# Kernel optimization log

Measured on AMD Instinct MI355X. Metric: run time of the kernel, lower is better.

The kernel has to match this reference:

```python
import jax, jax.numpy as jnp
import numpy as np

D = 1024       # d_model
H = 16         # total heads
HD = 64        # k_dim per head
HL = 8         # local heads (block-local attention)
STRIDE = 128   # block size
C = 32         # summary columns per block for global heads
DFF = 4096
EPS = 1e-6
NEG = -1e9


def layernorm(x, g, b):
    mu = jnp.mean(x, axis=-1, keepdims=True)
    var = jnp.mean(jnp.square(x - mu), axis=-1, keepdims=True)
    return g * (x - mu) / jnp.sqrt(var + EPS) + b


def setup_inputs() -> dict:
    key = jax.random.key(0)
    ks = jax.random.split(key, 16)
    B, S = 4, 4096
    s = 0.02
    inp = {
        "src": jax.random.normal(ks[0], (B, S, D), jnp.float32),
        "input_mask": jnp.ones((B, S), dtype=bool),
        "Wq": jax.random.normal(ks[1], (D, H * HD), jnp.float32) * s,
        "bq": jnp.zeros((H * HD,), jnp.float32),
        "Wk": jax.random.normal(ks[2], (D, H * HD), jnp.float32) * s,
        "bk": jnp.zeros((H * HD,), jnp.float32),
        "Wv": jax.random.normal(ks[3], (D, H * HD), jnp.float32) * s,
        "bv": jnp.zeros((H * HD,), jnp.float32),
        "Wo": jax.random.normal(ks[4], (H * HD, D), jnp.float32) * s,
        "bo": jnp.zeros((D,), jnp.float32),
        "ln1_g": jnp.ones((D,), jnp.float32),
        "ln1_b": jnp.zeros((D,), jnp.float32),
        "W1": jax.random.normal(ks[5], (D, DFF), jnp.float32) * s,
        "b1": jnp.zeros((DFF,), jnp.float32),
        "W2": jax.random.normal(ks[6], (DFF, D), jnp.float32) * s,
        "b2": jnp.zeros((D,), jnp.float32),
        "ln2_g": jnp.ones((D,), jnp.float32),
        "ln2_b": jnp.zeros((D,), jnp.float32),
    }
    return inp


def sparse_attention(src, input_mask, Wq, bq, Wk, bk, Wv, bv, Wo, bo):
    B, S, _ = src.shape
    nb = S // STRIDE
    scale = HD ** -0.5
    q = (src @ Wq + bq).reshape(B, S, H, HD)
    k = (src @ Wk + bk).reshape(B, S, H, HD)
    v = (src @ Wv + bv).reshape(B, S, H, HD)

    # ---- local heads: attend within their own block of length STRIDE ----
    ql = q[:, :, :HL].reshape(B, nb, STRIDE, HL, HD)
    kl = k[:, :, :HL].reshape(B, nb, STRIDE, HL, HD)
    vl = v[:, :, :HL].reshape(B, nb, STRIDE, HL, HD)
    sl = jnp.einsum('bnqhd,bnkhd->bnhqk', ql, kl) * scale
    mloc = input_mask.reshape(B, nb, 1, 1, STRIDE)
    sl = jnp.where(mloc, sl, NEG)
    al = jax.nn.softmax(sl, axis=-1)
    ol = jnp.einsum('bnhqk,bnkhd->bnqhd', al, vl).reshape(B, S, HL, HD)

    # ---- global heads: attend to last C positions of every block (fixed pattern) ----
    idx = np.nonzero(np.arange(S) % STRIDE >= STRIDE - C)[0]  # static, nb*C keys
    kg = k[:, idx, HL:]                        # [B, nb*C, HG, HD]
    vg = v[:, idx, HL:]
    sg = jnp.einsum('bqhd,bkhd->bhqk', q[:, :, HL:], kg) * scale
    mg = input_mask[:, idx][:, None, None, :]
    sg = jnp.where(mg, sg, NEG)
    ag = jax.nn.softmax(sg, axis=-1)
    og = jnp.einsum('bhqk,bkhd->bqhd', ag, vg)  # [B, S, HG, HD]

    out = jnp.concatenate([ol, og], axis=2).reshape(B, S, H * HD)
    return out @ Wo + bo


def reference(src, input_mask, Wq, bq, Wk, bk, Wv, bv, Wo, bo,
              ln1_g, ln1_b, W1, b1, W2, b2, ln2_g, ln2_b):
    temp = sparse_attention(src, input_mask, Wq, bq, Wk, bk, Wv, bv, Wo, bo)
    attn = layernorm(src + temp, ln1_g, ln1_b)
    ffn = jax.nn.relu(attn @ W1 + b1) @ W2 + b2
    state = layernorm(attn + ffn, ln2_g, ln2_b)
    return state
```

## Files before the change

### kernel.cpp

```cpp
#include <hip/hip_runtime.h>
#include <hip/hip_bf16.h>
#include <stdint.h>


typedef unsigned short bf16_t;
typedef __attribute__((ext_vector_type(8))) short short8;
typedef __attribute__((ext_vector_type(4))) float v4f;

static __device__ __forceinline__ unsigned short f2b(float f) {
    unsigned int x = __float_as_uint(f);
    x += 0x7fffu + ((x >> 16) & 1u);
    return (unsigned short)(x >> 16);
}
static __device__ __forceinline__ float b2f(unsigned short u) {
    return __uint_as_float(((unsigned int)u) << 16);
}

static __device__ __forceinline__ void gload16(const void* g, void* l) {
    __builtin_amdgcn_global_load_lds(
        (const __attribute__((address_space(1))) uint32_t*)g,
        (__attribute__((address_space(3))) uint32_t*)l, 16, 0, 0);
}

template<int N>
static __device__ __forceinline__ void vmwait() {
    asm volatile("s_waitcnt vmcnt(%0)" :: "n"(N) : "memory");
}
static __device__ __forceinline__ void lgkmwait0() {
    asm volatile("s_waitcnt lgkmcnt(0)" ::: "memory");
}


__global__ __launch_bounds__(256) void transpose_convert(
    const float* __restrict__ W, bf16_t* __restrict__ Wt, int K, int N) {
    __shared__ float tile[32][33];
    int n0 = blockIdx.x * 32, k0 = blockIdx.y * 32;
    int tx = threadIdx.x, ty = threadIdx.y;
    for (int i = ty; i < 32; i += 8)
        tile[i][tx] = W[(size_t)(k0 + i) * N + n0 + tx];
    __syncthreads();
    for (int i = ty; i < 32; i += 8)
        Wt[(size_t)(n0 + i) * K + k0 + tx] = f2b(tile[tx][i]);
}

__global__ __launch_bounds__(256) void f32_to_bf16_vec(
    const float* __restrict__ in, bf16_t* __restrict__ out, int n4) {
    int i = blockIdx.x * blockDim.x + threadIdx.x;
    if (i >= n4) return;
    float4 v = ((const float4*)in)[i];
    uint2 p;
    p.x = (unsigned)f2b(v.x) | ((unsigned)f2b(v.y) << 16);
    p.y = (unsigned)f2b(v.z) | ((unsigned)f2b(v.w) << 16);
    ((uint2*)out)[i] = p;
}

template<bool GLOBAL>
__global__ __launch_bounds__(256) void v_transpose(
    const bf16_t* __restrict__ qkv, bf16_t* __restrict__ vt, int ntok) {
    __shared__ bf16_t tile[4096];
    int tb = blockIdx.x, h = blockIdx.y, b = blockIdx.z;
    int t = threadIdx.x;
    size_t src = (size_t)b * 4096 * 3072 + (size_t)(GLOBAL ? h + 8 : h) * 64 + 2048;
    for (int u = t; u < 512; u += 256) {
        int row = u >> 3, g = u & 7;
        int lt = tb * 64 + row;
        int tok = GLOBAL ? ((lt >> 5) * 128 + 96 + (lt & 31)) : lt;
        short8 vrow = *(const short8*)(qkv + src + (size_t)tok * 3072 + g * 8);
        *(short8*)&tile[(row * 8 + (g ^ (row >> 3))) * 8] = vrow;
    }
    __syncthreads();
    for (int u = t; u < 512; u += 256) {
        int d = u >> 3, t8g = u & 7;
        short8 vcol;
#pragma unroll
        for (int j = 0; j < 8; ++j) {
            int row = t8g * 8 + j;
            vcol[j] = tile[(row * 8 + ((d >> 3) ^ (row >> 3))) * 8 + (d & 7)];
        }
        *(short8*)(vt + ((size_t)(b * 8 + h) * 64 + d) * ntok + (size_t)tb * 64 + t8g * 8) = vcol;
    }
}

template<int BN>
__global__ __launch_bounds__(512, 2) void gemm_bt(
    const bf16_t* __restrict__ A, const bf16_t* __restrict__ Bt,
    const float* __restrict__ bias, const float* __restrict__ bias2,
    const float* __restrict__ bias3, const float* __restrict__ resf,
    const bf16_t* __restrict__ resb, float* __restrict__ Cf,
    bf16_t* __restrict__ Cb, int N, int K, int relu) {
    constexpr int N_REP = BN / 64;
    constexpr int BLD = BN / 128;
    constexpr int LPT = 2 + BLD;
    constexpr int ASH = 8192;
    constexpr int TSH = ASH + BN * 32;
    __shared__ bf16_t lds[4][TSH];

    int t = threadIdx.x;
    int lane = t & 63;
    int wave = t >> 6;
    int wm = (wave >> 2) * 128;
    int wn = (wave & 3) * (BN / 4);
    int m0 = blockIdx.x * 256, n0 = blockIdx.y * BN;

    size_t aoff[2]; int adst[2];
#pragma unroll
    for (int p = 0; p < 2; ++p) {
        int u = p * 512 + t;
        int row = ((u >> 6) << 4) + (lane & 15);
        int kk = ((u >> 4) & 3) * 8;
        aoff[p] = (size_t)(m0 + row) * K + kk;
        adst[p] = (u & ~63) * 8;
    }
    size_t boff[BLD]; int bdst[BLD];
#pragma unroll
    for (int p = 0; p < BLD; ++p) {
        int u = p * 512 + t;
        int row = ((u >> 6) << 4) + (lane & 15);
        int kk = ((u >> 4) & 3) * 8;
        boff[p] = (size_t)(n0 + row) * K + kk;
        bdst[p] = (u & ~63) * 8;
    }

    auto stage = [&](int buf, int kt) {
        int k0 = kt * 32;
#pragma unroll
        for (int p = 0; p < 2; ++p)
            gload16(A + aoff[p] + k0, &lds[buf][adst[p]]);
#pragma unroll
        for (int p = 0; p < BLD; ++p)
            gload16(Bt + boff[p] + k0, &lds[buf][ASH + bdst[p]]);
    };

    v4f acc[8][N_REP];
#pragma unroll
    for (int i = 0; i < 8; ++i)
#pragma unroll
        for (int j = 0; j < N_REP; ++j) acc[i][j] = {0.f, 0.f, 0.f, 0.f};

    int NT = K >> 5;
    stage(0, 0); stage(1, 1); stage(2, 2);

    int aro = (wm >> 4) * 512 + lane * 8;
    int bro = ASH + (wn >> 4) * 512 + lane * 8;

    short8 fA0[8], fB0[N_REP], fA1[8], fB1[N_REP];

    auto prep = [&](int it, short8 (&gA)[8], short8 (&gB)[N_REP]) {
        if (it + 1 < NT) {
            if (it + 2 < NT) vmwait<LPT>();
            else vmwait<0>();
            __builtin_amdgcn_s_barrier();
            __builtin_amdgcn_sched_barrier(0);
            int nb = (it + 1) & 3;
#pragma unroll
            for (int i = 0; i < 8; ++i)
                gA[i] = *(const short8*)&lds[nb][aro + i * 512];
#pragma unroll
            for (int j = 0; j < N_REP; ++j)
                gB[j] = *(const short8*)&lds[nb][bro + j * 512];
            if (it + 3 < NT) stage((it + 3) & 3, it + 3);
            __builtin_amdgcn_sched_barrier(0);
        }
    };
    auto mstep = [&](short8 (&gA)[8], short8 (&gB)[N_REP]) {
        __builtin_amdgcn_s_setprio(1);
#pragma unroll
        for (int i = 0; i < 8; ++i)
#pragma unroll
            for (int j = 0; j < N_REP; ++j)
                acc[i][j] = __builtin_amdgcn_mfma_f32_16x16x32_bf16(gA[i], gB[j], acc[i][j], 0, 0, 0);
        __builtin_amdgcn_s_setprio(0);
    };

    vmwait<2 * LPT>();
    __builtin_amdgcn_s_barrier();
    __builtin_amdgcn_sched_barrier(0);
#pragma unroll
    for (int i = 0; i < 8; ++i) fA0[i] = *(const short8*)&lds[0][aro + i * 512];
#pragma unroll
    for (int j = 0; j < N_REP; ++j) fB0[j] = *(const short8*)&lds[0][bro + j * 512];

    for (int it = 0; it < NT; it += 2) {
        prep(it, fA1, fB1);
        mstep(fA0, fB0);
        prep(it + 1, fA0, fB0);
        mstep(fA1, fB1);
    }

    int qrow = (lane >> 4) * 4;
    int c15 = lane & 15;
#pragma unroll
    for (int i = 0; i < 8; ++i) {
#pragma unroll
        for (int j = 0; j < N_REP; ++j) {
            int col = n0 + wn + j * 16 + c15;
            float bval;
            if (bias2) {
                int seg = col >> 10;
                const float* bp = seg == 0 ? bias : (seg == 1 ? bias2 : bias3);
                bval = bp[col & 1023];
            } else {
                bval = bias[col];
            }
#pragma unroll
            for (int r = 0; r < 4; ++r) {
                int row = m0 + wm + i * 16 + qrow + r;
                size_t idx = (size_t)row * N + col;
                float val = acc[i][j][r] + bval;
                if (resf) val += resf[idx];
                if (resb) val += b2f(resb[idx]);
                if (relu) val = fmaxf(val, 0.f);
                if (Cf) Cf[idx] = val;
                if (Cb) Cb[idx] = f2b(val);
            }
        }
    }
}

template<int NCHUNK, bool GLOBAL>
__global__ __launch_bounds__(256) void mfma_attn(
    const bf16_t* __restrict__ qkv, const bf16_t* __restrict__ vt,
    bf16_t* __restrict__ o, int head_base) {
    __shared__ bf16_t buf[32768];
    bf16_t* ldsQ = buf;
    bf16_t* ldsP = buf;
    constexpr int KB = 8192, VB = 20480;

    int qc = blockIdx.x, hh = blockIdx.y, b = blockIdx.z;
    int h = head_base + hh;
    int t = threadIdx.x, lane = t & 63, w = t >> 6;
    int quad = lane >> 4, c15 = lane & 15;
    size_t base = (size_t)b * 4096 * 3072 + (size_t)h * 64;
    const int NTOK = GLOBAL ? 1024 : 4096;
    size_t vtbase = (size_t)(b * 8 + hh) * 64 * NTOK + (GLOBAL ? 0 : (size_t)qc * 128);
    const int CADV = (GLOBAL ? 256 : 64) * 3072;

    size_t koff[2]; int kdst[2];
#pragma unroll
    for (int p = 0; p < 2; ++p) {
        int u = p * 256 + t;
        int s = u >> 8;
        int kl = ((u >> 6) & 3) * 16 + (lane & 15);
        int dk = s * 32 + ((lane >> 4) & 3) * 8;
        int tok0 = GLOBAL ? ((kl >> 5) * 128 + 96 + (kl & 31)) : (qc * 128 + kl);
        koff[p] = base + 1024 + (size_t)tok0 * 3072 + dk;
        kdst[p] = KB + (u & ~63) * 8;
    }
    size_t voff[2]; int vdst[2];
#pragma unroll
    for (int p = 0; p < 2; ++p) {
        int u = p * 256 + t;
        int dd = ((u >> 6) & 3) * 16 + (lane & 15);
        int kl = (u >> 8) * 32 + ((lane >> 4) & 3) * 8;
        voff[p] = vtbase + (size_t)dd * NTOK + kl;
        vdst[p] = VB + (u & ~63) * 8;
    }

    auto stage = [&](int c) {
        int q = c % 3;
        size_t ka = (size_t)c * CADV;
        size_t va = (size_t)c * 64;
#pragma unroll
        for (int p = 0; p < 2; ++p)
            gload16(qkv + koff[p] + ka, buf + kdst[p] + q * 4096);
#pragma unroll
        for (int p = 0; p < 2; ++p)
            gload16(vt + voff[p] + va, buf + vdst[p] + q * 4096);
    };

#pragma unroll
    for (int u = t; u < 1024; u += 256) {
        int s = u >> 9, mt = (u >> 6) & 7, qq = (u >> 4) & 3, ll = u & 15;
        int tok = qc * 128 + mt * 16 + ll;
        gload16(qkv + base + (size_t)tok * 3072 + s * 32 + qq * 8, ldsQ + (u & ~63) * 8);
    }
    stage(0);
    stage(1);
    vmwait<8>();
    __builtin_amdgcn_s_barrier();

    short8 fQ[2][2];
#pragma unroll
    for (int i = 0; i < 2; ++i)
#pragma unroll
        for (int s = 0; s < 2; ++s)
            fQ[i][s] = *(const short8*)(ldsQ + (s * 512 + (w * 2 + i) * 64 + lane) * 8);
    lgkmwait0();
    __builtin_amdgcn_sched_barrier(0);

    v4f oacc[2][4];
    float lacc[2][4];
#pragma unroll
    for (int i = 0; i < 2; ++i)
#pragma unroll
        for (int n = 0; n < 4; ++n) oacc[i][n] = {0.f, 0.f, 0.f, 0.f};
#pragma unroll
    for (int i = 0; i < 2; ++i)
#pragma unroll
        for (int r = 0; r < 4; ++r) lacc[i][r] = 0.f;

    for (int c = 0; c < NCHUNK; ++c) {
        if (c + 1 < NCHUNK) vmwait<4>();
        else vmwait<0>();
        __builtin_amdgcn_s_barrier();
        __builtin_amdgcn_sched_barrier(0);
        if (c + 2 < NCHUNK) stage(c + 2);

        const bf16_t* Kq = buf + KB + (c % 3) * 4096;
        const bf16_t* Vq = buf + VB + (c % 3) * 4096;

        v4f sacc[2][4];
#pragma unroll
        for (int i = 0; i < 2; ++i)
#pragma unroll
            for (int j = 0; j < 4; ++j) sacc[i][j] = {0.f, 0.f, 0.f, 0.f};
        __builtin_amdgcn_s_setprio(1);
#pragma unroll
        for (int s = 0; s < 2; ++s)
#pragma unroll
            for (int j = 0; j < 4; ++j) {
                short8 fK = *(const short8*)(Kq + (s * 256 + j * 64 + lane) * 8);
#pragma unroll
                for (int i = 0; i < 2; ++i)
                    sacc[i][j] = __builtin_amdgcn_mfma_f32_16x16x32_bf16(fQ[i][s], fK, sacc[i][j], 0, 0, 0);
            }
        __builtin_amdgcn_s_setprio(0);

#pragma unroll
        for (int i = 0; i < 2; ++i) {
            float rs[4] = {0.f, 0.f, 0.f, 0.f};
#pragma unroll
            for (int j = 0; j < 4; ++j)
#pragma unroll
                for (int r = 0; r < 4; ++r) {
                    float p = __expf(sacc[i][j][r] * 0.125f);
                    sacc[i][j][r] = p;
                    rs[r] += p;
                }
#pragma unroll
            for (int m = 1; m < 16; m <<= 1)
#pragma unroll
                for (int r = 0; r < 4; ++r) rs[r] += __shfl_xor(rs[r], m);
#pragma unroll
            for (int r = 0; r < 4; ++r) lacc[i][r] += rs[r];
#pragma unroll
            for (int j = 0; j < 4; ++j) {
                int tt = j >> 1;
                int qq = (2 * j + (c15 >> 3)) & 3;
#pragma unroll
                for (int r = 0; r < 4; ++r) {
                    int slot = (quad * 4 + r) ^ qq;
                    int unit = (w * 2 + tt) * 128 + i * 64 + qq * 16 + slot;
                    ldsP[unit * 8 + (c15 & 7)] = f2b(sacc[i][j][r]);
                }
            }
        }

        __builtin_amdgcn_s_setprio(1);
#pragma unroll
        for (int tt = 0; tt < 2; ++tt) {
            short8 fP[2];
#pragma unroll
            for (int i = 0; i < 2; ++i)
                fP[i] = *(const short8*)(ldsP + ((w * 2 + tt) * 128 + i * 64
                              + quad * 16 + (c15 ^ quad)) * 8);
#pragma unroll
            for (int n = 0; n < 4; ++n) {
                short8 fV = *(const short8*)(Vq + (tt * 256 + n * 64 + lane) * 8);
#pragma unroll
                for (int i = 0; i < 2; ++i)
                    oacc[i][n] = __builtin_amdgcn_mfma_f32_16x16x32_bf16(fP[i], fV, oacc[i][n], 0, 0, 0);
            }
        }
        __builtin_amdgcn_s_setprio(0);
    }

#pragma unroll
    for (int i = 0; i < 2; ++i)
#pragma unroll
        for (int r = 0; r < 4; ++r) {
            int row = qc * 128 + (w * 2 + i) * 16 + quad * 4 + r;
            float inv = 1.f / lacc[i][r];
            bf16_t* orow = o + ((size_t)b * 4096 + row) * 1024 + h * 64;
#pragma unroll
            for (int n = 0; n < 4; ++n)
                orow[n * 16 + c15] = f2b(oacc[i][n][r] * inv);
        }
}

__global__ __launch_bounds__(256) void ln_kernel(
    const float* x, const float* g, const float* bta,
    float* outf, bf16_t* outb) {
    int row = blockIdx.x, t = threadIdx.x;
    const float4 vv = ((const float4*)(x + (size_t)row * 1024))[t];
    float s = vv.x + vv.y + vv.z + vv.w;
    float ss = vv.x * vv.x + vv.y * vv.y + vv.z * vv.z + vv.w * vv.w;
    for (int off = 32; off > 0; off >>= 1) {
        s += __shfl_down(s, off);
        ss += __shfl_down(ss, off);
    }
    __shared__ float red[8];
    int wave = t >> 6;
    if ((t & 63) == 0) { red[wave] = s; red[wave + 4] = ss; }
    __syncthreads();
    float ts = red[0] + red[1] + red[2] + red[3];
    float tss = red[4] + red[5] + red[6] + red[7];
    float mu = ts * (1.f / 1024.f);
    float var = tss * (1.f / 1024.f) - mu * mu;
    float rstd = rsqrtf(var + 1e-6f);
    float4 gv = ((const float4*)g)[t];
    float4 bv = ((const float4*)bta)[t];
    float4 ov;
    ov.x = (vv.x - mu) * rstd * gv.x + bv.x;
    ov.y = (vv.y - mu) * rstd * gv.y + bv.y;
    ov.z = (vv.z - mu) * rstd * gv.z + bv.z;
    ov.w = (vv.w - mu) * rstd * gv.w + bv.w;
    if (outf) ((float4*)(outf + (size_t)row * 1024))[t] = ov;
    if (outb) {
        uint2 pk;
        pk.x = (unsigned)f2b(ov.x) | ((unsigned)f2b(ov.y) << 16);
        pk.y = (unsigned)f2b(ov.z) | ((unsigned)f2b(ov.w) << 16);
        ((uint2*)(outb + (size_t)row * 1024))[t] = pk;
    }
}

extern "C" void kernel_launch(void* const* d_in, const int* in_sizes, int n_in,
                              void* d_out, int out_size, void* d_ws, size_t ws_size,
                              hipStream_t stream) {
    const float* src = (const float*)d_in[0];
    const float* Wq = (const float*)d_in[2];  const float* bq = (const float*)d_in[3];
    const float* Wk = (const float*)d_in[4];  const float* bk = (const float*)d_in[5];
    const float* Wv = (const float*)d_in[6];  const float* bv = (const float*)d_in[7];
    const float* Wo = (const float*)d_in[8];  const float* bo = (const float*)d_in[9];
    const float* g1 = (const float*)d_in[10]; const float* be1 = (const float*)d_in[11];
    const float* W1 = (const float*)d_in[12]; const float* b1 = (const float*)d_in[13];
    const float* W2 = (const float*)d_in[14]; const float* b2 = (const float*)d_in[15];
    const float* g2 = (const float*)d_in[16]; const float* be2 = (const float*)d_in[17];
    float* out = (float*)d_out;
    char* ws = (char*)d_ws;
    const size_t MB = 1ull << 20;

    bf16_t* xb    = (bf16_t*)(ws + 0 * MB);
    bf16_t* ob    = (bf16_t*)(ws + 0 * MB);
    bf16_t* alnb  = (bf16_t*)(ws + 0 * MB);
    bf16_t* qkv   = (bf16_t*)(ws + 32 * MB);
    bf16_t* hb    = (bf16_t*)(ws + 32 * MB);
    bf16_t* vt_l  = (bf16_t*)(ws + 128 * MB);
    bf16_t* vt_g  = (bf16_t*)(ws + 144 * MB);
    bf16_t* wqkvt = (bf16_t*)(ws + 152 * MB);
    bf16_t* wot   = (bf16_t*)(ws + 158 * MB);
    bf16_t* w1t   = (bf16_t*)(ws + 160 * MB);
    bf16_t* w2t   = (bf16_t*)(ws + 168 * MB);

    dim3 tb(32, 8);
    transpose_convert<<<dim3(32, 32), tb, 0, stream>>>(Wq, wqkvt, 1024, 1024);
    transpose_convert<<<dim3(32, 32), tb, 0, stream>>>(Wk, wqkvt + 1024 * 1024, 1024, 1024);
    transpose_convert<<<dim3(32, 32), tb, 0, stream>>>(Wv, wqkvt + 2 * 1024 * 1024, 1024, 1024);
    transpose_convert<<<dim3(32, 32), tb, 0, stream>>>(Wo, wot, 1024, 1024);
    transpose_convert<<<dim3(128, 32), tb, 0, stream>>>(W1, w1t, 1024, 4096);
    transpose_convert<<<dim3(32, 128), tb, 0, stream>>>(W2, w2t, 4096, 1024);
    f32_to_bf16_vec<<<16384, 256, 0, stream>>>(src, xb, 4194304);

    gemm_bt<256><<<dim3(64, 12), 512, 0, stream>>>(xb, wqkvt, bq, bk, bv,
        nullptr, nullptr, nullptr, qkv, 3072, 1024, 0);

    v_transpose<false><<<dim3(64, 8, 4), 256, 0, stream>>>(qkv, vt_l, 4096);
    v_transpose<true ><<<dim3(16, 8, 4), 256, 0, stream>>>(qkv, vt_g, 1024);

    mfma_attn<2,  false><<<dim3(32, 8, 4), 256, 0, stream>>>(qkv, vt_l, ob, 0);
    mfma_attn<16, true ><<<dim3(32, 8, 4), 256, 0, stream>>>(qkv, vt_g, ob, 8);

    gemm_bt<256><<<dim3(64, 4), 512, 0, stream>>>(ob, wot, bo, nullptr, nullptr,
        src, nullptr, out, nullptr, 1024, 1024, 0);
    ln_kernel<<<16384, 256, 0, stream>>>(out, g1, be1, nullptr, alnb);

    gemm_bt<256><<<dim3(64, 16), 512, 0, stream>>>(alnb, w1t, b1, nullptr, nullptr,
        nullptr, nullptr, nullptr, hb, 4096, 1024, 1);
    gemm_bt<256><<<dim3(64, 4), 512, 0, stream>>>(hb, w2t, b2, nullptr, nullptr,
        nullptr, alnb, out, nullptr, 1024, 4096, 0);
    ln_kernel<<<16384, 256, 0, stream>>>(out, g2, be2, out, nullptr);

    (void)in_sizes; (void)n_in; (void)out_size; (void)ws_size;
}
```

Baseline: 933.3 us.

## Restructure GEMM main loop into double-buffered 64-wide K steps with interleaved loads

Replaces the 4-stage, 32-wide-K ring buffer GEMM with a 2-buffer scheme where each 64-wide K tile is split into four sub-phases. Each sub-phase loads part of the A or B fragments, issues the next tile's global-to-LDS copies, then runs half of the MFMAs. The aim is to spread memory traffic evenly across the MFMA work and keep the LDS footprint small. In exchange it adds several extra barriers per iteration and a shallower prefetch depth, which can expose global load latency. On the last iteration it also issues redundant loads for a clamped tile index.

```diff
diff --git a/kernel.cpp b/kernel.cpp
--- a/kernel.cpp
+++ b/kernel.cpp
@@ -81,118 +81,140 @@
     }
 }
 
-template<int BN>
-__global__ __launch_bounds__(512, 2) void gemm_bt(
+__global__ __launch_bounds__(512, 2) void gemm_bt256(
     const bf16_t* __restrict__ A, const bf16_t* __restrict__ Bt,
     const float* __restrict__ bias, const float* __restrict__ bias2,
     const float* __restrict__ bias3, const float* __restrict__ resf,
     const bf16_t* __restrict__ resb, float* __restrict__ Cf,
     bf16_t* __restrict__ Cb, int N, int K, int relu) {
-    constexpr int N_REP = BN / 64;
-    constexpr int BLD = BN / 128;
-    constexpr int LPT = 2 + BLD;
-    constexpr int ASH = 8192;
-    constexpr int TSH = ASH + BN * 32;
-    __shared__ bf16_t lds[4][TSH];
+    __shared__ bf16_t lds[2][32768];
 
     int t = threadIdx.x;
     int lane = t & 63;
     int wave = t >> 6;
     int wm = (wave >> 2) * 128;
-    int wn = (wave & 3) * (BN / 4);
-    int m0 = blockIdx.x * 256, n0 = blockIdx.y * BN;
-
-    size_t aoff[2]; int adst[2];
+    int wn = (wave & 3) * 64;
+    int m0 = blockIdx.x * 256, n0 = blockIdx.y * 256;
+
+    size_t aoff[2], boff[2]; int sdst[2];
 #pragma unroll
     for (int p = 0; p < 2; ++p) {
         int u = p * 512 + t;
         int row = ((u >> 6) << 4) + (lane & 15);
         int kk = ((u >> 4) & 3) * 8;
         aoff[p] = (size_t)(m0 + row) * K + kk;
-        adst[p] = (u & ~63) * 8;
-    }
-    size_t boff[BLD]; int bdst[BLD];
-#pragma unroll
-    for (int p = 0; p < BLD; ++p) {
-        int u = p * 512 + t;
-        int row = ((u >> 6) << 4) + (lane & 15);
-        int kk = ((u >> 4) & 3) * 8;
         boff[p] = (size_t)(n0 + row) * K + kk;
-        bdst[p] = (u & ~63) * 8;
-    }
-
-    auto stage = [&](int buf, int kt) {
-        int k0 = kt * 32;
+        sdst[p] = (u & ~63) * 8;
+    }
+
+    auto stageA = [&](int bufi, int ks, int kt) {
+        int k0 = kt * 64 + ks * 32;
 #pragma unroll
         for (int p = 0; p < 2; ++p)
-            gload16(A + aoff[p] + k0, &lds[buf][adst[p]]);
-#pragma unroll
-        for (int p = 0; p < BLD; ++p)
-            gload16(Bt + boff[p] + k0, &lds[buf][ASH + bdst[p]]);
+            gload16(A + aoff[p] + k0, &lds[bufi][ks * 8192 + sdst[p]]);
     };
-
-    v4f acc[8][N_REP];
+    auto stageB = [&](int bufi, int ks, int kt) {
+        int k0 = kt * 64 + ks * 32;
+#pragma unroll
+        for (int p = 0; p < 2; ++p)
+            gload16(Bt + boff[p] + k0, &lds[bufi][16384 + ks * 8192 + sdst[p]]);
+    };
+
+    v4f acc[8][4];
 #pragma unroll
     for (int i = 0; i < 8; ++i)
 #pragma unroll
-        for (int j = 0; j < N_REP; ++j) acc[i][j] = {0.f, 0.f, 0.f, 0.f};
-
-    int NT = K >> 5;
-    stage(0, 0); stage(1, 1); stage(2, 2);
-
-    int aro = (wm >> 4) * 512 + lane * 8;
-    int bro = ASH + (wn >> 4) * 512 + lane * 8;
-
-    short8 fA0[8], fB0[N_REP], fA1[8], fB1[N_REP];
-
-    auto prep = [&](int it, short8 (&gA)[8], short8 (&gB)[N_REP]) {
-        if (it + 1 < NT) {
-            if (it + 2 < NT) vmwait<LPT>();
-            else vmwait<0>();
-            __builtin_amdgcn_s_barrier();
-            __builtin_amdgcn_sched_barrier(0);
-            int nb = (it + 1) & 3;
-#pragma unroll
-            for (int i = 0; i < 8; ++i)
-                gA[i] = *(const short8*)&lds[nb][aro + i * 512];
-#pragma unroll
-            for (int j = 0; j < N_REP; ++j)
-                gB[j] = *(const short8*)&lds[nb][bro + j * 512];
-            if (it + 3 < NT) stage((it + 3) & 3, it + 3);
-            __builtin_amdgcn_sched_barrier(0);
-        }
-    };
-    auto mstep = [&](short8 (&gA)[8], short8 (&gB)[N_REP]) {
+        for (int j = 0; j < 4; ++j) acc[i][j] = {0.f, 0.f, 0.f, 0.f};
+
+    int NT = K >> 6;
+    int aro = ((wave >> 2) * 8) * 512 + lane * 8;
+    int brd = 16384 + ((wave & 3) * 4) * 512 + lane * 8;
+
+    stageA(0, 0, 0); stageB(0, 0, 0); stageA(0, 1, 0); stageB(0, 1, 0);
+    vmwait<4>();
+    __builtin_amdgcn_s_barrier();
+
+    for (int t0 = 0; t0 < NT; ++t0) {
+        int cur = t0 & 1, nxt = cur ^ 1;
+        int ktn = t0 + 1 < NT ? t0 + 1 : NT - 1;
+        short8 fa[8], fb0, fb1, fb2, fb3;
+
+#pragma unroll
+        for (int i = 0; i < 8; ++i)
+            fa[i] = *(const short8*)&lds[cur][aro + i * 512];
+        fb0 = *(const short8*)&lds[cur][brd + 0 * 512];
+        fb1 = *(const short8*)&lds[cur][brd + 1 * 512];
+        stageA(nxt, 0, ktn);
+        __builtin_amdgcn_s_barrier();
+        lgkmwait0();
+        __builtin_amdgcn_sched_barrier(0);
         __builtin_amdgcn_s_setprio(1);
 #pragma unroll
+        for (int i = 0; i < 8; ++i) {
+            acc[i][0] = __builtin_amdgcn_mfma_f32_16x16x32_bf16(fa[i], fb0, acc[i][0], 0, 0, 0);
+            acc[i][1] = __builtin_amdgcn_mfma_f32_16x16x32_bf16(fa[i], fb1, acc[i][1], 0, 0, 0);
+        }
+        __builtin_amdgcn_s_setprio(0);
+        __builtin_amdgcn_s_barrier();
+
+        fb2 = *(const short8*)&lds[cur][brd + 2 * 512];
+        fb3 = *(const short8*)&lds[cur][brd + 3 * 512];
+        stageB(nxt, 0, ktn);
+        __builtin_amdgcn_s_barrier();
+        lgkmwait0();
+        __builtin_amdgcn_sched_barrier(0);
+        __builtin_amdgcn_s_setprio(1);
+#pragma unroll
+        for (int i = 0; i < 8; ++i) {
+            acc[i][2] = __builtin_amdgcn_mfma_f32_16x16x32_bf16(fa[i], fb2, acc[i][2], 0, 0, 0);
+            acc[i][3] = __builtin_amdgcn_mfma_f32_16x16x32_bf16(fa[i], fb3, acc[i][3], 0, 0, 0);
+        }
+        __builtin_amdgcn_s_setprio(0);
+        vmwait<4>();
+        __builtin_amdgcn_s_barrier();
+
+#pragma unroll
         for (int i = 0; i < 8; ++i)
-#pragma unroll
-            for (int j = 0; j < N_REP; ++j)
-                acc[i][j] = __builtin_amdgcn_mfma_f32_16x16x32_bf16(gA[i], gB[j], acc[i][j], 0, 0, 0);
+            fa[i] = *(const short8*)&lds[cur][8192 + aro + i * 512];
+        fb0 = *(const short8*)&lds[cur][8192 + brd + 0 * 512];
+        fb1 = *(const short8*)&lds[cur][8192 + brd + 1 * 512];
+        stageA(nxt, 1, ktn);
+        __builtin_amdgcn_s_barrier();
+        lgkmwait0();
+        __builtin_amdgcn_sched_barrier(0);
+        __builtin_amdgcn_s_setprio(1);
+#pragma unroll
+        for (int i = 0; i < 8; ++i) {
+            acc[i][0] = __builtin_amdgcn_mfma_f32_16x16x32_bf16(fa[i], fb0, acc[i][0], 0, 0, 0);
+            acc[i][1] = __builtin_amdgcn_mfma_f32_16x16x32_bf16(fa[i], fb1, acc[i][1], 0, 0, 0);
+        }
         __builtin_amdgcn_s_setprio(0);
-    };
-
-    vmwait<2 * LPT>();
-    __builtin_amdgcn_s_barrier();
-    __builtin_amdgcn_sched_barrier(0);
-#pragma unroll
-    for (int i = 0; i < 8; ++i) fA0[i] = *(const short8*)&lds[0][aro + i * 512];
-#pragma unroll
-    for (int j = 0; j < N_REP; ++j) fB0[j] = *(const short8*)&lds[0][bro + j * 512];
-
-    for (int it = 0; it < NT; it += 2) {
-        prep(it, fA1, fB1);
-        mstep(fA0, fB0);
-        prep(it + 1, fA0, fB0);
-        mstep(fA1, fB1);
-    }
+        __builtin_amdgcn_s_barrier();
+
+        fb2 = *(const short8*)&lds[cur][8192 + brd + 2 * 512];
+        fb3 = *(const short8*)&lds[cur][8192 + brd + 3 * 512];
+        stageB(nxt, 1, ktn);
+        __builtin_amdgcn_s_barrier();
+        lgkmwait0();
+        __builtin_amdgcn_sched_barrier(0);
+        __builtin_amdgcn_s_setprio(1);
+#pragma unroll
+        for (int i = 0; i < 8; ++i) {
+            acc[i][2] = __builtin_amdgcn_mfma_f32_16x16x32_bf16(fa[i], fb2, acc[i][2], 0, 0, 0);
+            acc[i][3] = __builtin_amdgcn_mfma_f32_16x16x32_bf16(fa[i], fb3, acc[i][3], 0, 0, 0);
+        }
+        __builtin_amdgcn_s_setprio(0);
+        vmwait<4>();
+        __builtin_amdgcn_s_barrier();
+    }
+    vmwait<0>();
 
     int qrow = (lane >> 4) * 4;
     int c15 = lane & 15;
 #pragma unroll
     for (int i = 0; i < 8; ++i) {
 #pragma unroll
-        for (int j = 0; j < N_REP; ++j) {
+        for (int j = 0; j < 4; ++j) {
             int col = n0 + wn + j * 16 + c15;
             float bval;
             if (bias2) {
@@ -461,7 +483,7 @@
     transpose_convert<<<dim3(32, 128), tb, 0, stream>>>(W2, w2t, 4096, 1024);
     f32_to_bf16_vec<<<16384, 256, 0, stream>>>(src, xb, 4194304);
 
-    gemm_bt<256><<<dim3(64, 12), 512, 0, stream>>>(xb, wqkvt, bq, bk, bv,
+    gemm_bt256<<<dim3(64, 12), 512, 0, stream>>>(xb, wqkvt, bq, bk, bv,
         nullptr, nullptr, nullptr, qkv, 3072, 1024, 0);
 
     v_transpose<false><<<dim3(64, 8, 4), 256, 0, stream>>>(qkv, vt_l, 4096);
@@ -470,13 +492,13 @@
     mfma_attn<2,  false><<<dim3(32, 8, 4), 256, 0, stream>>>(qkv, vt_l, ob, 0);
     mfma_attn<16, true ><<<dim3(32, 8, 4), 256, 0, stream>>>(qkv, vt_g, ob, 8);
 
-    gemm_bt<256><<<dim3(64, 4), 512, 0, stream>>>(ob, wot, bo, nullptr, nullptr,
+    gemm_bt256<<<dim3(64, 4), 512, 0, stream>>>(ob, wot, bo, nullptr, nullptr,
         src, nullptr, out, nullptr, 1024, 1024, 0);
     ln_kernel<<<16384, 256, 0, stream>>>(out, g1, be1, nullptr, alnb);
 
-    gemm_bt<256><<<dim3(64, 16), 512, 0, stream>>>(alnb, w1t, b1, nullptr, nullptr,
+    gemm_bt256<<<dim3(64, 16), 512, 0, stream>>>(alnb, w1t, b1, nullptr, nullptr,
         nullptr, nullptr, nullptr, hb, 4096, 1024, 1);
-    gemm_bt<256><<<dim3(64, 4), 512, 0, stream>>>(hb, w2t, b2, nullptr, nullptr,
+    gemm_bt256<<<dim3(64, 4), 512, 0, stream>>>(hb, w2t, b2, nullptr, nullptr,
         nullptr, alnb, out, nullptr, 1024, 4096, 0);
     ln_kernel<<<16384, 256, 0, stream>>>(out, g2, be2, out, nullptr);
 
```

Result: no change. 922.0 us (-1.2%).
